# Kernel optimization log

Measured on AMD Instinct MI355X. Metric: run time of the kernel, lower is better.

The kernel has to match this reference:

```python
import jax, jax.numpy as jnp
import numpy as np

EMBED = 1024
HEADS = 16
HEAD_DIM = EMBED // HEADS
HIDDEN = 4096
EPS = 1e-5


def setup_inputs() -> dict:
    key = jax.random.key(0)
    ks = jax.random.split(key, 16)
    s_e = 1.0 / np.sqrt(EMBED)
    s_h = 1.0 / np.sqrt(HIDDEN)
    return {
        "x": jax.random.normal(ks[0], (8, 1024, EMBED), dtype=jnp.float32),
        "ln1_g": jnp.ones((EMBED,), jnp.float32),
        "ln1_b": jnp.zeros((EMBED,), jnp.float32),
        "ln2_g": jnp.ones((EMBED,), jnp.float32),
        "ln2_b": jnp.zeros((EMBED,), jnp.float32),
        "wq": jax.random.uniform(ks[1], (EMBED, EMBED), jnp.float32, -s_e, s_e),
        "bq": jax.random.uniform(ks[2], (EMBED,), jnp.float32, -s_e, s_e),
        "wk": jax.random.uniform(ks[3], (EMBED, EMBED), jnp.float32, -s_e, s_e),
        "bk": jax.random.uniform(ks[4], (EMBED,), jnp.float32, -s_e, s_e),
        "wv": jax.random.uniform(ks[5], (EMBED, EMBED), jnp.float32, -s_e, s_e),
        "bv": jax.random.uniform(ks[6], (EMBED,), jnp.float32, -s_e, s_e),
        "wo": jax.random.uniform(ks[7], (EMBED, EMBED), jnp.float32, -s_e, s_e),
        "bo": jax.random.uniform(ks[8], (EMBED,), jnp.float32, -s_e, s_e),
        "w1": jax.random.uniform(ks[9], (EMBED, HIDDEN), jnp.float32, -s_e, s_e),
        "b1": jax.random.uniform(ks[10], (HIDDEN,), jnp.float32, -s_e, s_e),
        "w2": jax.random.uniform(ks[11], (HIDDEN, EMBED), jnp.float32, -s_h, s_h),
        "b2": jax.random.uniform(ks[12], (EMBED,), jnp.float32, -s_h, s_h),
    }


def _layernorm(x, g, b):
    mu = jnp.mean(x, axis=-1, keepdims=True)
    var = jnp.mean((x - mu) ** 2, axis=-1, keepdims=True)
    return (x - mu) * jax.lax.rsqrt(var + EPS) * g + b


def reference(x, ln1_g, ln1_b, ln2_g, ln2_b, wq, bq, wk, bk, wv, bv, wo, bo, w1, b1, w2, b2):
    B, N, E = x.shape
    scale = HEAD_DIM ** (-0.5)
    # --- attention sublayer (pre-norm) ---
    h = _layernorm(x, ln1_g, ln1_b)
    q = (h @ wq + bq).reshape(B, N, HEADS, HEAD_DIM).transpose(0, 2, 1, 3) * scale
    k = (h @ wk + bk).reshape(B, N, HEADS, HEAD_DIM).transpose(0, 2, 1, 3)
    v = (h @ wv + bv).reshape(B, N, HEADS, HEAD_DIM).transpose(0, 2, 1, 3)
    scores = jnp.einsum("bhqd,bhkd->bhqk", q, k)
    attn = jax.nn.softmax(scores, axis=-1)
    ctx = jnp.einsum("bhqk,bhkd->bhqd", attn, v)
    ctx = ctx.transpose(0, 2, 1, 3).reshape(B, N, E)
    x = x + (ctx @ wo + bo)
    # --- FFN sublayer (pre-norm) ---
    h2 = _layernorm(x, ln2_g, ln2_b)
    ff = jax.nn.relu(h2 @ w1 + b1) @ w2 + b2
    return x + ff
```

## Files before the change

### kernel.cpp

```cpp
#include <hip/hip_runtime.h>
#include <hip/hip_bf16.h>

typedef __attribute__((ext_vector_type(4))) float f32x4;
typedef __attribute__((ext_vector_type(16))) float f32x16;
typedef __attribute__((ext_vector_type(8))) __bf16 bf16x8;
typedef __attribute__((ext_vector_type(4))) __bf16 bf16x4;
typedef __attribute__((ext_vector_type(4))) unsigned int u32x4;

static constexpr int E    = 1024;
static constexpr int TOK  = 8192;
static constexpr int HID  = 4096;

#define DEVINL __device__ __forceinline__

DEVINL void gload16(const void* g, void* l) {
  __builtin_amdgcn_global_load_lds((__attribute__((address_space(1))) void*)g,
                                   (__attribute__((address_space(3))) void*)l, 16, 0, 0);
}

#define ABAR()  asm volatile("s_barrier" ::: "memory")
#define AVM(n)  asm volatile("s_waitcnt vmcnt(" #n ")" ::: "memory")
#define ALGKM0() asm volatile("s_waitcnt lgkmcnt(0)")
#define CVTPK(dst, lo, hi) asm("v_cvt_pk_bf16_f32 %0, %1, %2" : "=v"(dst) : "v"(lo), "v"(hi))
#define PLSWAP(a, b) asm("v_permlane32_swap_b32 %0, %1" : "+v"(a), "+v"(b))

template <int N> DEVINL void avm() {
  if constexpr (N == 0)      asm volatile("s_waitcnt vmcnt(0)" ::: "memory");
  else if constexpr (N == 2) asm volatile("s_waitcnt vmcnt(2)" ::: "memory");
  else if constexpr (N == 6) asm volatile("s_waitcnt vmcnt(6)" ::: "memory");
  else if constexpr (N == 8) asm volatile("s_waitcnt vmcnt(8)" ::: "memory");
  else if constexpr (N == 9) asm volatile("s_waitcnt vmcnt(9)" ::: "memory");
  else                       asm volatile("s_waitcnt vmcnt(0)" ::: "memory");
}

__global__ __launch_bounds__(256) void wconv6ln_kernel(const float* __restrict__ wq,
                                                       const float* __restrict__ wk,
                                                       const float* __restrict__ wv,
                                                       const float* __restrict__ wo,
                                                       const float* __restrict__ w1,
                                                       const float* __restrict__ w2,
                                                       __bf16* __restrict__ Wqkv,
                                                       __bf16* __restrict__ Wot,
                                                       __bf16* __restrict__ W1t,
                                                       __bf16* __restrict__ W2t,
                                                       const float* __restrict__ X,
                                                       const float* __restrict__ g,
                                                       const float* __restrict__ be,
                                                       __bf16* __restrict__ O) {
  const int id = blockIdx.x;
  const int t  = threadIdx.x;
  __shared__ float tile[32][33];
  __shared__ float red[8];

  if (id >= 12288) {
    const long row = id - 12288;
    float4 v = *(const float4*)&X[row * E + t * 4];
    float s  = v.x + v.y + v.z + v.w;
    float ss = v.x * v.x + v.y * v.y + v.z * v.z + v.w * v.w;
#pragma unroll
    for (int off = 32; off; off >>= 1) {
      s  += __shfl_down(s, off);
      ss += __shfl_down(ss, off);
    }
    const int w = t >> 6;
    if ((t & 63) == 0) { red[w] = s; red[4 + w] = ss; }
    __syncthreads();
    s  = red[0] + red[1] + red[2] + red[3];
    ss = red[4] + red[5] + red[6] + red[7];
    const float mean = s * (1.0f / E);
    const float var  = ss * (1.0f / E) - mean * mean;
    const float rstd = rsqrtf(var + 1e-5f);
    float4 gv = *(const float4*)&g[t * 4];
    float4 bv = *(const float4*)&be[t * 4];
    bf16x4 o;
    o[0] = (__bf16)((v.x - mean) * rstd * gv.x + bv.x);
    o[1] = (__bf16)((v.y - mean) * rstd * gv.y + bv.y);
    o[2] = (__bf16)((v.z - mean) * rstd * gv.z + bv.z);
    o[3] = (__bf16)((v.w - mean) * rstd * gv.w + bv.w);
    *(bf16x4*)&O[row * E + t * 4] = o;
    return;
  }

  const float* W; __bf16* Wt; int K, N, lid;
  if (id < 1024)      { W = wq; Wt = Wqkv;                K = 1024; N = 1024; lid = id; }
  else if (id < 2048) { W = wk; Wt = Wqkv + 1024 * 1024;  K = 1024; N = 1024; lid = id - 1024; }
  else if (id < 3072) { W = wv; Wt = Wqkv + 2048 * 1024;  K = 1024; N = 1024; lid = id - 2048; }
  else if (id < 4096) { W = wo; Wt = Wot;                 K = 1024; N = 1024; lid = id - 3072; }
  else if (id < 8192) { W = w1; Wt = W1t;                 K = 1024; N = 4096; lid = id - 4096; }
  else                { W = w2; Wt = W2t;                 K = 4096; N = 1024; lid = id - 8192; }
  const int nx = N >> 5;
  const long n0 = (long)(lid % nx) * 32;
  const long k0 = (long)(lid / nx) * 32;

  const int r  = t >> 3;
  const int c4 = (t & 7) * 4;
  float4 v = *(const float4*)&W[(k0 + r) * N + n0 + c4];
  tile[r][c4 + 0] = v.x; tile[r][c4 + 1] = v.y;
  tile[r][c4 + 2] = v.z; tile[r][c4 + 3] = v.w;
  __syncthreads();
  bf16x4 o;
#pragma unroll
  for (int i = 0; i < 4; ++i) o[i] = (__bf16)tile[c4 + i][r];
  *(bf16x4*)&Wt[(n0 + r) * K + k0 + c4] = o;
}

__global__ __launch_bounds__(256) void ln_kernel(const float* __restrict__ X,
                                                 const float* __restrict__ g,
                                                 const float* __restrict__ be,
                                                 __bf16* __restrict__ O) {
  const int t = threadIdx.x;
  const long row = blockIdx.x;
  float4 v = *(const float4*)&X[row * E + t * 4];
  float s  = v.x + v.y + v.z + v.w;
  float ss = v.x * v.x + v.y * v.y + v.z * v.z + v.w * v.w;
#pragma unroll
  for (int off = 32; off; off >>= 1) {
    s  += __shfl_down(s, off);
    ss += __shfl_down(ss, off);
  }
  __shared__ float red[8];
  const int w = t >> 6;
  if ((t & 63) == 0) { red[w] = s; red[4 + w] = ss; }
  __syncthreads();
  s  = red[0] + red[1] + red[2] + red[3];
  ss = red[4] + red[5] + red[6] + red[7];
  const float mean = s * (1.0f / E);
  const float var  = ss * (1.0f / E) - mean * mean;
  const float rstd = rsqrtf(var + 1e-5f);
  float4 gv = *(const float4*)&g[t * 4];
  float4 bv = *(const float4*)&be[t * 4];
  bf16x4 o;
  o[0] = (__bf16)((v.x - mean) * rstd * gv.x + bv.x);
  o[1] = (__bf16)((v.y - mean) * rstd * gv.y + bv.y);
  o[2] = (__bf16)((v.z - mean) * rstd * gv.z + bv.z);
  o[3] = (__bf16)((v.w - mean) * rstd * gv.w + bv.w);
  *(bf16x4*)&O[row * E + t * 4] = o;
}

template <bool RELU, bool RESID, bool OUTBF, int NB>
__global__ __launch_bounds__(512, 2) void gemm8p_kernel(const __bf16* __restrict__ A,
                                                        const __bf16* __restrict__ Bt,
                                                        const float* __restrict__ bias0,
                                                        const float* __restrict__ bias1,
                                                        const float* __restrict__ bias2,
                                                        const float* resid,
                                                        void* Cout, void* Cout2,
                                                        int M, int N, int K, int KLD) {
  extern __shared__ char lds[];
  const int tid  = threadIdx.x;
  const int lane = tid & 63;
  const int l15  = lane & 15;
  const int kp   = lane >> 4;
  const int wid  = tid >> 6;
  const int wr   = wid >> 2;
  const int wc   = wid & 3;

  const int gx   = gridDim.x, gy = gridDim.y;
  const int nwg  = gx * gy * gridDim.z;
  const int flat = blockIdx.x + gx * (blockIdx.y + gy * blockIdx.z);
  const int swz  = (flat & 7) * (nwg >> 3) + (flat >> 3);
  const int bx   = swz % gx;
  const int by   = (swz / gx) % gy;
  const int bz   = swz / (gx * gy);
  const long brow = (long)by * 256;
  const long bcol = (long)bx * 256;
  const long koff = (long)bz * K;

  const __bf16* Ab = A  + brow * KLD + koff;
  const __bf16* Bb = Bt + bcol * KLD + koff;
  void* Cdst = bz ? Cout2 : Cout;
  const int NT = K >> 6;

  auto stageU = [&](const __bf16* Gb, int rc0, int k0, int dstOff) {
#pragma unroll
    for (int i = 0; i < 2; ++i) {
      const int c = i * 512 + tid;
      const int r = c >> 3;
      const int p = (c & 7) ^ (r & 7);
      gload16(Gb + (long)(rc0 + r) * KLD + k0 + p * 8, lds + dstOff + c * 16);
    }
  };

  f32x4 acc[8][4];
  const f32x4 z4 = {0.f, 0.f, 0.f, 0.f};
#pragma unroll
  for (int m = 0; m < 8; ++m)
#pragma unroll
    for (int n = 0; n < 4; ++n) acc[m][n] = z4;

  bf16x8 af[4][2], bh0[2][2], bh1[2][2];

  auto readA = [&](int off) {
#pragma unroll
    for (int mm = 0; mm < 4; ++mm)
#pragma unroll
      for (int kk = 0; kk < 2; ++kk) {
        const int lr = mm * 32 + wr * 16 + l15;
        const int p  = ((kk << 2) + kp) ^ (lr & 7);
        af[mm][kk] = *(const bf16x8*)(lds + off + lr * 128 + p * 16);
      }
  };
  auto readB = [&](int off, bf16x8 (*bf)[2]) {
#pragma unroll
    for (int nn = 0; nn < 2; ++nn)
#pragma unroll
      for (int kk = 0; kk < 2; ++kk) {
        const int lc = nn * 64 + wc * 16 + l15;
        const int p  = ((kk << 2) + kp) ^ (lc & 7);
        bf[nn][kk] = *(const bf16x8*)(lds + off + lc * 128 + p * 16);
      }
  };
  auto quad = [&](int mb, int nb, bf16x8 (*bf)[2]) {
    __builtin_amdgcn_s_setprio(1);
#pragma unroll
    for (int kk = 0; kk < 2; ++kk)
#pragma unroll
      for (int mm = 0; mm < 4; ++mm)
#pragma unroll
        for (int nn = 0; nn < 2; ++nn)
          acc[mb + mm][nb + nn] = __builtin_amdgcn_mfma_f32_16x16x32_bf16(
              af[mm][kk], bf[nn][kk], acc[mb + mm][nb + nn], 0, 0, 0);
    __builtin_amdgcn_s_setprio(0);
  };

  stageU(Ab, 0,   0, 0);
  stageU(Bb, 0,   0, 32768);
  stageU(Bb, 128, 0, 49152);
  stageU(Ab, 128, 0, 16384);
  stageU(Ab, 0,   64, 65536 + 0);
  stageU(Bb, 0,   64, 65536 + 32768);
  stageU(Bb, 128, 64, 65536 + 49152);
  avm<6>();
  ABAR();

  for (int t = 0; t < NT; ++t) {
    const int cb  = (t & 1) ? 65536 : 0;
    const int nb1 = cb ^ 65536;
    const int k1 = (t + 1 < NT) ? ((t + 1) << 6) : 0;
    const int k2 = (t + 2 < NT) ? ((t + 2) << 6) : 0;

    readA(cb + 0);
    readB(cb + 32768, bh0);
    stageU(Ab, 128, k1, nb1 + 16384);
    ABAR(); ALGKM0();
    quad(0, 0, bh0);
    ABAR();

    readB(cb + 49152, bh1);
    stageU(Ab, 0, k2, cb + 0);
    ABAR(); ALGKM0();
    quad(0, 2, bh1);
    ABAR();

    readA(cb + 16384);
    stageU(Bb, 0, k2, cb + 32768);
    ABAR(); ALGKM0();
    quad(4, 0, bh0);
    ABAR();

    stageU(Bb, 128, k2, cb + 49152);
    avm<6>();
    ABAR();
    quad(4, 2, bh1);
    ABAR();
  }
  avm<0>();

#pragma unroll
  for (int m = 0; m < 8; ++m) {
#pragma unroll
    for (int n = 0; n < 4; ++n) {
      const long col = bcol + n * 64 + wc * 16 + l15;
      float bb;
      if (NB == 3) {
        const float* bp = (col < 1024) ? bias0 : ((col < 2048) ? bias1 : bias2);
        bb = bp[col & 1023];
      } else if (NB == 1) {
        bb = bias0[col];
      } else {
        bb = 0.f;
      }
#pragma unroll
      for (int j = 0; j < 4; ++j) {
        const long row = brow + m * 32 + wr * 16 + (lane >> 4) * 4 + j;
        float val = acc[m][n][j] + bb;
        if (RELU) val = fmaxf(val, 0.f);
        const long idx = row * N + col;
        if (RESID) val += resid[idx];
        if (OUTBF) ((__bf16*)Cdst)[idx] = (__bf16)val;
        else       ((float*)Cdst)[idx]  = val;
      }
    }
  }
}

template <int BM_, int DEPTH, bool RELU, bool RESID, bool OUTBF, int NB>
__global__ __launch_bounds__(512, 2) void gemmk_kernel(const __bf16* __restrict__ A,
                                                       const __bf16* __restrict__ Bt,
                                                       const float* __restrict__ bias0,
                                                       const float* __restrict__ bias1,
                                                       const float* __restrict__ bias2,
                                                       const float* resid,
                                                       void* Cout, void* Cout2,
                                                       int M, int N, int K, int KLD) {
  extern __shared__ char lds[];
  constexpr int MF    = BM_ / 32;
  constexpr int ABYT  = BM_ * 64;
  constexpr int TILEB = ABYT + 16384;
  constexpr int AL    = BM_ / 128;
  constexpr int TL    = AL + 2;
  constexpr int W     = (DEPTH - 2) * TL;

  const int tid  = threadIdx.x;
  const int lane = tid & 63;
  const int l15  = lane & 15;
  const int kp   = lane >> 4;
  const int wid  = tid >> 6;
  const int wr   = wid >> 2;
  const int wc   = wid & 3;

  const int gx   = gridDim.x, gy = gridDim.y;
  const int nwg  = gx * gy * gridDim.z;
  const int flat = blockIdx.x + gx * (blockIdx.y + gy * blockIdx.z);
  const int swz  = (flat & 7) * (nwg >> 3) + (flat >> 3);
  const int bx   = swz % gx;
  const int by   = (swz / gx) % gy;
  const int bz   = swz / (gx * gy);
  const long brow = (long)by * BM_;
  const long bcol = (long)bx * 256;
  const long koff = (long)bz * K;

  const __bf16* Ab = A  + brow * KLD + koff;
  const __bf16* Bb = Bt + bcol * KLD + koff;
  void* Cdst = bz ? Cout2 : Cout;
  const int NT = K >> 5;

  auto stageA = [&](int k0, char* dst) {
#pragma unroll
    for (int i = 0; i < AL; ++i) {
      const int c = i * 512 + tid;
      const int r = c >> 2;
      const int p = (c & 3) ^ ((r >> 1) & 3);
      gload16(Ab + (long)r * KLD + k0 + p * 8, dst + c * 16);
    }
  };
  auto stageB = [&](int k0, char* dst) {
#pragma unroll
    for (int i = 0; i < 2; ++i) {
      const int c = i * 512 + tid;
      const int r = c >> 2;
      const int p = (c & 3) ^ ((r >> 1) & 3);
      gload16(Bb + (long)r * KLD + k0 + p * 8, dst + c * 16);
    }
  };

  f32x4 acc[MF][4];
  const f32x4 z4 = {0.f, 0.f, 0.f, 0.f};
#pragma unroll
  for (int m = 0; m < MF; ++m)
#pragma unroll
    for (int n = 0; n < 4; ++n) acc[m][n] = z4;

#pragma unroll
  for (int pt = 0; pt < DEPTH - 1; ++pt) {
    stageA(pt * 32, lds + pt * TILEB);
    stageB(pt * 32, lds + pt * TILEB + ABYT);
  }

  bf16x8 af[4], bfr[4];

  for (int t = 0; t < NT; ++t) {
    const int cb = t % DEPTH;
    const int sb = (t + DEPTH - 1) % DEPTH;
    const char* Ac = lds + cb * TILEB;
    const char* Bc = Ac + ABYT;
    char* An = lds + sb * TILEB;
    const int kt = (t + DEPTH - 1 < NT) ? ((t + DEPTH - 1) << 5) : 0;

    avm<W>();
    ABAR();

#pragma unroll
    for (int m = 0; m < 4; ++m) {
      const int row = m * 32 + wr * 16 + l15;
      af[m] = *(const bf16x8*)(Ac + row * 64 + (kp ^ ((row >> 1) & 3)) * 16);
    }
#pragma unroll
    for (int n = 0; n < 4; ++n) {
      const int col = n * 64 + wc * 16 + l15;
      bfr[n] = *(const bf16x8*)(Bc + col * 64 + (kp ^ ((col >> 1) & 3)) * 16);
    }
    stageA(kt, An);
    stageB(kt, An + ABYT);
    __builtin_amdgcn_s_setprio(1);
#pragma unroll
    for (int m = 0; m < 4; ++m)
#pragma unroll
      for (int n = 0; n < 4; ++n)
        acc[m][n] = __builtin_amdgcn_mfma_f32_16x16x32_bf16(af[m], bfr[n], acc[m][n], 0, 0, 0);
    __builtin_amdgcn_s_setprio(0);
  }
  avm<0>();

#pragma unroll
  for (int m = 0; m < MF; ++m) {
#pragma unroll
    for (int n = 0; n < 4; ++n) {
      const long col = bcol + n * 64 + wc * 16 + l15;
      float bb;
      if (NB == 3) {
        const float* bp = (col < 1024) ? bias0 : ((col < 2048) ? bias1 : bias2);
        bb = bp[col & 1023];
      } else if (NB == 1) {
        bb = bias0[col];
      } else {
        bb = 0.f;
      }
#pragma unroll
      for (int j = 0; j < 4; ++j) {
        const long row = brow + m * 32 + wr * 16 + (lane >> 4) * 4 + j;
        float val = acc[m][n][j] + bb;
        if (RELU) val = fmaxf(val, 0.f);
        const long idx = row * N + col;
        if (RESID) val += resid[idx];
        if (OUTBF) ((__bf16*)Cdst)[idx] = (__bf16)val;
        else       ((float*)Cdst)[idx]  = val;
      }
    }
  }
}

__global__ __launch_bounds__(256, 3) void attn_kernel(const __bf16* __restrict__ QKV,
                                                      __bf16* __restrict__ Og) {
  __shared__ __align__(16) __bf16 Qs[128 * 64];
  __shared__ __align__(16) __bf16 Ks[2][64 * 64];
  __shared__ __align__(16) __bf16 Vt[2][64 * 64];

  const int QSTR = 3072;
  const int t    = threadIdx.x;
  const int lane = t & 63;
  const int w    = t >> 6;
  const int l31  = lane & 31;
  const int h    = lane >> 5;
  const int b    = blockIdx.y >> 4;
  const int hh   = blockIdx.y & 15;
  const long row0 = (long)b * 1024 + (long)blockIdx.x * 128;
  const long kvrow0 = (long)b * 1024;
  const int colQ = hh * 64;
  const int colK = colQ + 1024;
  const int colV = colQ + 2048;

#pragma unroll
  for (int j = 0; j < 4; ++j) {
    const int c = j * 256 + t;
    const int r = c >> 3;
    const int p = (c & 7) ^ (r & 7);
    gload16(QKV + (row0 + r) * QSTR + colQ + p * 8, (char*)Qs + c * 16);
  }
#pragma unroll
  for (int j = 0; j < 2; ++j) {
    const int c = j * 256 + t;
    const int r = c >> 3;
    const int p = (c & 7) ^ (r & 7);
    gload16(QKV + (kvrow0 + r) * QSTR + colK + p * 8, (char*)Ks[0] + c * 16);
  }
  bf16x8 vv[2];
#pragma unroll
  for (int j = 0; j < 2; ++j) {
    const int c = j * 256 + t;
    const int key = c >> 3, dc = c & 7;
    vv[j] = *(const bf16x8*)(QKV + (kvrow0 + key) * QSTR + colV + dc * 8);
  }
  AVM(0);
#pragma unroll
  for (int j = 0; j < 2; ++j) {
    const int c = j * 256 + t;
    const int key = c >> 3, dc = c & 7;
#pragma unroll
    for (int e = 0; e < 8; ++e) {
      const int d = dc * 8 + e;
      *(__bf16*)((char*)Vt[0] + d * 128 + (((key >> 3) ^ dc) * 16) + (key & 7) * 2) = vv[j][e];
    }
  }
  __syncthreads();

  bf16x8 bq[4];
  {
    const int qrow = w * 32 + l31;
#pragma unroll
    for (int kk = 0; kk < 4; ++kk) {
      const int p = (kk * 2 + h) ^ (qrow & 7);
      bq[kk] = *(const bf16x8*)((const char*)Qs + qrow * 128 + p * 16);
    }
  }

  f32x16 ctx0, ctx1;
#pragma unroll
  for (int r = 0; r < 16; ++r) { ctx0[r] = 0.f; ctx1[r] = 0.f; }
  float m = -INFINITY, l = 0.f;

  for (int kb = 0; kb < 16; ++kb) {
    const int cur = kb & 1, nxt = cur ^ 1;
    const int kb1 = (kb + 1 < 16) ? kb + 1 : kb;
    const long kr1 = kvrow0 + kb1 * 64;

#pragma unroll
    for (int j = 0; j < 2; ++j) {
      const int c = j * 256 + t;
      const int key = c >> 3, dc = c & 7;
      vv[j] = *(const bf16x8*)(QKV + (kr1 + key) * QSTR + colV + dc * 8);
    }
#pragma unroll
    for (int j = 0; j < 2; ++j) {
      const int c = j * 256 + t;
      const int r = c >> 3;
      const int p = (c & 7) ^ (r & 7);
      gload16(QKV + (kr1 + r) * QSTR + colK + p * 8, (char*)Ks[nxt] + c * 16);
    }

    f32x16 s0, s1;
#pragma unroll
    for (int r = 0; r < 16; ++r) { s0[r] = 0.f; s1[r] = 0.f; }
    __builtin_amdgcn_s_setprio(1);
#pragma unroll
    for (int kk = 0; kk < 4; ++kk) {
      const int pce = kk * 2 + h;
      const int p0i = pce ^ (l31 & 7);
      bf16x8 ak0 = *(const bf16x8*)((const char*)Ks[cur] + l31 * 128 + p0i * 16);
      bf16x8 ak1 = *(const bf16x8*)((const char*)Ks[cur] + (32 + l31) * 128 + p0i * 16);
      s0 = __builtin_amdgcn_mfma_f32_32x32x16_bf16(ak0, bq[kk], s0, 0, 0, 0);
      s1 = __builtin_amdgcn_mfma_f32_32x32x16_bf16(ak1, bq[kk], s1, 0, 0, 0);
    }
    __builtin_amdgcn_s_setprio(0);

    float mx = s0[0];
#pragma unroll
    for (int r = 1; r < 16; ++r) mx = fmaxf(mx, s0[r]);
#pragma unroll
    for (int r = 0; r < 16; ++r) mx = fmaxf(mx, s1[r]);
    mx = fmaxf(mx, __shfl_xor(mx, 32));

    if (!__all(mx - m <= 64.f)) {
      const float mn = fmaxf(m, mx);
      const float corr = __expf((m - mn) * 0.125f);
      l *= corr;
#pragma unroll
      for (int r = 0; r < 16; ++r) { ctx0[r] *= corr; ctx1[r] *= corr; }
      m = mn;
    }
    f32x16 p0, p1;
    float rs = 0.f;
#pragma unroll
    for (int r = 0; r < 16; ++r) { p0[r] = __expf((s0[r] - m) * 0.125f); rs += p0[r]; }
#pragma unroll
    for (int r = 0; r < 16; ++r) { p1[r] = __expf((s1[r] - m) * 0.125f); rs += p1[r]; }
    rs += __shfl_xor(rs, 32);
    l += rs;

    AVM(2);
#pragma unroll
    for (int j = 0; j < 2; ++j) {
      const int c = j * 256 + t;
      const int key = c >> 3, dc = c & 7;
#pragma unroll
      for (int e = 0; e < 8; ++e) {
        const int d = dc * 8 + e;
        *(__bf16*)((char*)Vt[nxt] + d * 128 + (((key >> 3) ^ dc) * 16) + (key & 7) * 2) = vv[j][e];
      }
    }

    bf16x8 paf[4];
#pragma unroll
    for (int ks = 0; ks < 4; ++ks) {
      const int base = (ks & 1) * 8;
      unsigned a0, a1, b0, b1;
      if (ks < 2) {
        CVTPK(a0, p0[base + 0], p0[base + 1]);
        CVTPK(b0, p0[base + 4], p0[base + 5]);
        CVTPK(a1, p0[base + 2], p0[base + 3]);
        CVTPK(b1, p0[base + 6], p0[base + 7]);
      } else {
        CVTPK(a0, p1[base + 0], p1[base + 1]);
        CVTPK(b0, p1[base + 4], p1[base + 5]);
        CVTPK(a1, p1[base + 2], p1[base + 3]);
        CVTPK(b1, p1[base + 6], p1[base + 7]);
      }
      PLSWAP(a0, b0);
      PLSWAP(a1, b1);
      u32x4 wv4; wv4[0] = a0; wv4[1] = a1; wv4[2] = b0; wv4[3] = b1;
      paf[ks] = __builtin_bit_cast(bf16x8, wv4);
    }

    __builtin_amdgcn_s_setprio(1);
#pragma unroll
    for (int ks = 0; ks < 4; ++ks) {
      const int pce = ks * 2 + h;
      bf16x8 av0 = *(const bf16x8*)((const char*)Vt[cur] + l31 * 128 + ((pce ^ (l31 >> 3)) * 16));
      bf16x8 av1 = *(const bf16x8*)((const char*)Vt[cur] + (32 + l31) * 128 + ((pce ^ (4 + (l31 >> 3))) * 16));
      ctx0 = __builtin_amdgcn_mfma_f32_32x32x16_bf16(av0, paf[ks], ctx0, 0, 0, 0);
      ctx1 = __builtin_amdgcn_mfma_f32_32x32x16_bf16(av1, paf[ks], ctx1, 0, 0, 0);
    }
    __builtin_amdgcn_s_setprio(0);

    __syncthreads();
  }

  const float inv = 1.0f / l;
  const long orow = row0 + w * 32 + l31;
#pragma unroll
  for (int f = 0; f < 2; ++f)
#pragma unroll
    for (int tq = 0; tq < 4; ++tq) {
      bf16x4 o;
#pragma unroll
      for (int e = 0; e < 4; ++e) {
        const float v = (f ? ctx1[tq * 4 + e] : ctx0[tq * 4 + e]) * inv;
        o[e] = (__bf16)v;
      }
      const int col = colQ + f * 32 + tq * 8 + h * 4;
      *(bf16x4*)&Og[orow * E + col] = o;
    }
}

extern "C" void kernel_launch(void* const* d_in, const int* in_sizes, int n_in,
                              void* d_out, int out_size, void* d_ws, size_t ws_size,
                              hipStream_t stream) {
  const float* x     = (const float*)d_in[0];
  const float* ln1g  = (const float*)d_in[1];
  const float* ln1b  = (const float*)d_in[2];
  const float* ln2g  = (const float*)d_in[3];
  const float* ln2b  = (const float*)d_in[4];
  const float* wq    = (const float*)d_in[5];
  const float* bq    = (const float*)d_in[6];
  const float* wk    = (const float*)d_in[7];
  const float* bk    = (const float*)d_in[8];
  const float* wv    = (const float*)d_in[9];
  const float* bv    = (const float*)d_in[10];
  const float* wo    = (const float*)d_in[11];
  const float* bo    = (const float*)d_in[12];
  const float* w1    = (const float*)d_in[13];
  const float* b1    = (const float*)d_in[14];
  const float* w2    = (const float*)d_in[15];
  const float* b2    = (const float*)d_in[16];
  float* out = (float*)d_out;

  char* ws = (char*)d_ws;
  const size_t MB = 1024 * 1024;
  __bf16* Wqkv = (__bf16*)(ws + 0 * MB);
  __bf16* Wot  = (__bf16*)(ws + 6 * MB);
  __bf16* W1t  = (__bf16*)(ws + 8 * MB);
  __bf16* W2t  = (__bf16*)(ws + 16 * MB);
  __bf16* h    = (__bf16*)(ws + 24 * MB);
  __bf16* qkv  = (__bf16*)(ws + 40 * MB);
  __bf16* ctx  = (__bf16*)(ws + 88 * MB);
  __bf16* ff1  = (__bf16*)(ws + 40 * MB);

  const dim3 blk(256);
  const dim3 blk512(512);
  const size_t GLDS8P  = 131072;
  const size_t GLDS128 = 5 * (128 * 64 + 16384);

  wconv6ln_kernel<<<20480, blk, 0, stream>>>(wq, wk, wv, wo, w1, w2,
                                             Wqkv, Wot, W1t, W2t,
                                             x, ln1g, ln1b, h);

  gemm8p_kernel<false, false, true, 3><<<dim3(3072 / 256, TOK / 256), blk512, GLDS8P, stream>>>(
      h, Wqkv, bq, bk, bv, nullptr, qkv, nullptr, TOK, 3072, E, E);

  attn_kernel<<<dim3(8, 128), blk, 0, stream>>>(qkv, ctx);

  gemmk_kernel<128, 5, false, true, false, 1><<<dim3(E / 256, TOK / 128), blk512, GLDS128, stream>>>(
      ctx, Wot, bo, nullptr, nullptr, x, out, nullptr, TOK, E, E, E);

  ln_kernel<<<TOK, blk, 0, stream>>>(out, ln2g, ln2b, h);

  gemm8p_kernel<true, false, true, 1><<<dim3(HID / 256, TOK / 256), blk512, GLDS8P, stream>>>(
      h, W1t, b1, nullptr, nullptr, nullptr, ff1, nullptr, TOK, HID, E, E);

  gemmk_kernel<128, 5, false, true, false, 1><<<dim3(E / 256, TOK / 128), blk512, GLDS128, stream>>>(
      ff1, W2t, b2, nullptr, nullptr, out, out, nullptr, TOK, E, HID, HID);
}
```

Baseline: 350.8 us.

## Replace gemmk with 128x256 eight-phase double-buffered GEMM using BK=64 quadrant schedule

Result: no change. 352.5 us (+0.5%).

```diff
diff --git a/kernel.cpp b/kernel.cpp
--- a/kernel.cpp
+++ b/kernel.cpp
@@ -27,9 +27,8 @@
 template <int N> DEVINL void avm() {
   if constexpr (N == 0)      asm volatile("s_waitcnt vmcnt(0)" ::: "memory");
   else if constexpr (N == 2) asm volatile("s_waitcnt vmcnt(2)" ::: "memory");
+  else if constexpr (N == 5) asm volatile("s_waitcnt vmcnt(5)" ::: "memory");
   else if constexpr (N == 6) asm volatile("s_waitcnt vmcnt(6)" ::: "memory");
-  else if constexpr (N == 8) asm volatile("s_waitcnt vmcnt(8)" ::: "memory");
-  else if constexpr (N == 9) asm volatile("s_waitcnt vmcnt(9)" ::: "memory");
   else                       asm volatile("s_waitcnt vmcnt(0)" ::: "memory");
 }
 
@@ -144,7 +143,7 @@
                                                         const float* __restrict__ bias1,
                                                         const float* __restrict__ bias2,
                                                         const float* resid,
-                                                        void* Cout, void* Cout2,
+                                                        void* Cout,
                                                         int M, int N, int K, int KLD) {
   extern __shared__ char lds[];
   const int tid  = threadIdx.x;
@@ -156,19 +155,16 @@
   const int wc   = wid & 3;
 
   const int gx   = gridDim.x, gy = gridDim.y;
-  const int nwg  = gx * gy * gridDim.z;
-  const int flat = blockIdx.x + gx * (blockIdx.y + gy * blockIdx.z);
+  const int nwg  = gx * gy;
+  const int flat = blockIdx.x + gx * blockIdx.y;
   const int swz  = (flat & 7) * (nwg >> 3) + (flat >> 3);
   const int bx   = swz % gx;
-  const int by   = (swz / gx) % gy;
-  const int bz   = swz / (gx * gy);
+  const int by   = swz / gx;
   const long brow = (long)by * 256;
   const long bcol = (long)bx * 256;
-  const long koff = (long)bz * K;
-
-  const __bf16* Ab = A  + brow * KLD + koff;
-  const __bf16* Bb = Bt + bcol * KLD + koff;
-  void* Cdst = bz ? Cout2 : Cout;
+
+  const __bf16* Ab = A  + brow * KLD;
+  const __bf16* Bb = Bt + bcol * KLD;
   const int NT = K >> 6;
 
   auto stageU = [&](const __bf16* Gb, int rc0, int k0, int dstOff) {
@@ -287,30 +283,23 @@
         if (RELU) val = fmaxf(val, 0.f);
         const long idx = row * N + col;
         if (RESID) val += resid[idx];
-        if (OUTBF) ((__bf16*)Cdst)[idx] = (__bf16)val;
-        else       ((float*)Cdst)[idx]  = val;
+        if (OUTBF) ((__bf16*)Cout)[idx] = (__bf16)val;
+        else       ((float*)Cout)[idx]  = val;
       }
     }
   }
 }
 
-template <int BM_, int DEPTH, bool RELU, bool RESID, bool OUTBF, int NB>
-__global__ __launch_bounds__(512, 2) void gemmk_kernel(const __bf16* __restrict__ A,
-                                                       const __bf16* __restrict__ Bt,
-                                                       const float* __restrict__ bias0,
-                                                       const float* __restrict__ bias1,
-                                                       const float* __restrict__ bias2,
-                                                       const float* resid,
-                                                       void* Cout, void* Cout2,
-                                                       int M, int N, int K, int KLD) {
+template <bool RELU, bool RESID, bool OUTBF, int NB>
+__global__ __launch_bounds__(512, 2) void gemm8h_kernel(const __bf16* __restrict__ A,
+                                                        const __bf16* __restrict__ Bt,
+                                                        const float* __restrict__ bias0,
+                                                        const float* __restrict__ bias1,
+                                                        const float* __restrict__ bias2,
+                                                        const float* resid,
+                                                        void* Cout,
+                                                        int M, int N, int K, int KLD) {
   extern __shared__ char lds[];
-  constexpr int MF    = BM_ / 32;
-  constexpr int ABYT  = BM_ * 64;
-  constexpr int TILEB = ABYT + 16384;
-  constexpr int AL    = BM_ / 128;
-  constexpr int TL    = AL + 2;
-  constexpr int W     = (DEPTH - 2) * TL;
-
   const int tid  = threadIdx.x;
   const int lane = tid & 63;
   const int l15  = lane & 15;
@@ -320,90 +309,121 @@
   const int wc   = wid & 3;
 
   const int gx   = gridDim.x, gy = gridDim.y;
-  const int nwg  = gx * gy * gridDim.z;
-  const int flat = blockIdx.x + gx * (blockIdx.y + gy * blockIdx.z);
+  const int nwg  = gx * gy;
+  const int flat = blockIdx.x + gx * blockIdx.y;
   const int swz  = (flat & 7) * (nwg >> 3) + (flat >> 3);
   const int bx   = swz % gx;
-  const int by   = (swz / gx) % gy;
-  const int bz   = swz / (gx * gy);
-  const long brow = (long)by * BM_;
+  const int by   = swz / gx;
+  const long brow = (long)by * 128;
   const long bcol = (long)bx * 256;
-  const long koff = (long)bz * K;
-
-  const __bf16* Ab = A  + brow * KLD + koff;
-  const __bf16* Bb = Bt + bcol * KLD + koff;
-  void* Cdst = bz ? Cout2 : Cout;
-  const int NT = K >> 5;
-
-  auto stageA = [&](int k0, char* dst) {
-#pragma unroll
-    for (int i = 0; i < AL; ++i) {
-      const int c = i * 512 + tid;
-      const int r = c >> 2;
-      const int p = (c & 3) ^ ((r >> 1) & 3);
-      gload16(Ab + (long)r * KLD + k0 + p * 8, dst + c * 16);
-    }
-  };
-  auto stageB = [&](int k0, char* dst) {
+
+  const __bf16* Ab = A  + brow * KLD;
+  const __bf16* Bb = Bt + bcol * KLD;
+  const int NT = K >> 6;
+
+  auto stageA = [&](int rc0, int k0, int dstOff) {
+    const int c = tid;
+    const int r = c >> 3;
+    const int p = (c & 7) ^ (r & 7);
+    gload16(Ab + (long)(rc0 + r) * KLD + k0 + p * 8, lds + dstOff + c * 16);
+  };
+  auto stageB = [&](int rc0, int k0, int dstOff) {
 #pragma unroll
     for (int i = 0; i < 2; ++i) {
       const int c = i * 512 + tid;
-      const int r = c >> 2;
-      const int p = (c & 3) ^ ((r >> 1) & 3);
-      gload16(Bb + (long)r * KLD + k0 + p * 8, dst + c * 16);
-    }
-  };
-
-  f32x4 acc[MF][4];
+      const int r = c >> 3;
+      const int p = (c & 7) ^ (r & 7);
+      gload16(Bb + (long)(rc0 + r) * KLD + k0 + p * 8, lds + dstOff + c * 16);
+    }
+  };
+
+  f32x4 acc[4][4];
   const f32x4 z4 = {0.f, 0.f, 0.f, 0.f};
 #pragma unroll
-  for (int m = 0; m < MF; ++m)
+  for (int m = 0; m < 4; ++m)
 #pragma unroll
     for (int n = 0; n < 4; ++n) acc[m][n] = z4;
 
-#pragma unroll
-  for (int pt = 0; pt < DEPTH - 1; ++pt) {
-    stageA(pt * 32, lds + pt * TILEB);
-    stageB(pt * 32, lds + pt * TILEB + ABYT);
-  }
-
-  bf16x8 af[4], bfr[4];
+  bf16x8 af[2][2], bh0[2][2], bh1[2][2];
+
+  auto readA = [&](int off) {
+#pragma unroll
+    for (int mm = 0; mm < 2; ++mm)
+#pragma unroll
+      for (int kk = 0; kk < 2; ++kk) {
+        const int lr = mm * 32 + wr * 16 + l15;
+        const int p  = ((kk << 2) + kp) ^ (lr & 7);
+        af[mm][kk] = *(const bf16x8*)(lds + off + lr * 128 + p * 16);
+      }
+  };
+  auto readB = [&](int off, bf16x8 (*bf)[2]) {
+#pragma unroll
+    for (int nn = 0; nn < 2; ++nn)
+#pragma unroll
+      for (int kk = 0; kk < 2; ++kk) {
+        const int lc = nn * 64 + wc * 16 + l15;
+        const int p  = ((kk << 2) + kp) ^ (lc & 7);
+        bf[nn][kk] = *(const bf16x8*)(lds + off + lc * 128 + p * 16);
+      }
+  };
+  auto quad = [&](int mb, int nb, bf16x8 (*bf)[2]) {
+    __builtin_amdgcn_s_setprio(1);
+#pragma unroll
+    for (int kk = 0; kk < 2; ++kk)
+#pragma unroll
+      for (int mm = 0; mm < 2; ++mm)
+#pragma unroll
+        for (int nn = 0; nn < 2; ++nn)
+          acc[mb + mm][nb + nn] = __builtin_amdgcn_mfma_f32_16x16x32_bf16(
+              af[mm][kk], bf[nn][kk], acc[mb + mm][nb + nn], 0, 0, 0);
+    __builtin_amdgcn_s_setprio(0);
+  };
+
+  stageA(0,   0, 0);
+  stageB(0,   0, 16384);
+  stageB(128, 0, 32768);
+  stageA(64,  0, 8192);
+  stageA(0,   64, 49152 + 0);
+  stageB(0,   64, 49152 + 16384);
+  stageB(128, 64, 49152 + 32768);
+  avm<5>();
+  ABAR();
 
   for (int t = 0; t < NT; ++t) {
-    const int cb = t % DEPTH;
-    const int sb = (t + DEPTH - 1) % DEPTH;
-    const char* Ac = lds + cb * TILEB;
-    const char* Bc = Ac + ABYT;
-    char* An = lds + sb * TILEB;
-    const int kt = (t + DEPTH - 1 < NT) ? ((t + DEPTH - 1) << 5) : 0;
-
-    avm<W>();
-    ABAR();
-
-#pragma unroll
-    for (int m = 0; m < 4; ++m) {
-      const int row = m * 32 + wr * 16 + l15;
-      af[m] = *(const bf16x8*)(Ac + row * 64 + (kp ^ ((row >> 1) & 3)) * 16);
-    }
-#pragma unroll
-    for (int n = 0; n < 4; ++n) {
-      const int col = n * 64 + wc * 16 + l15;
-      bfr[n] = *(const bf16x8*)(Bc + col * 64 + (kp ^ ((col >> 1) & 3)) * 16);
-    }
-    stageA(kt, An);
-    stageB(kt, An + ABYT);
-    __builtin_amdgcn_s_setprio(1);
-#pragma unroll
-    for (int m = 0; m < 4; ++m)
-#pragma unroll
-      for (int n = 0; n < 4; ++n)
-        acc[m][n] = __builtin_amdgcn_mfma_f32_16x16x32_bf16(af[m], bfr[n], acc[m][n], 0, 0, 0);
-    __builtin_amdgcn_s_setprio(0);
+    const int cb  = (t & 1) ? 49152 : 0;
+    const int nb1 = cb ^ 49152;
+    const int k1 = (t + 1 < NT) ? ((t + 1) << 6) : 0;
+    const int k2 = (t + 2 < NT) ? ((t + 2) << 6) : 0;
+
+    readA(cb + 0);
+    readB(cb + 16384, bh0);
+    stageA(64, k1, nb1 + 8192);
+    ABAR(); ALGKM0();
+    quad(0, 0, bh0);
+    ABAR();
+
+    readB(cb + 32768, bh1);
+    stageA(0, k2, cb + 0);
+    ABAR(); ALGKM0();
+    quad(0, 2, bh1);
+    ABAR();
+
+    readA(cb + 8192);
+    stageB(0, k2, cb + 16384);
+    ABAR(); ALGKM0();
+    quad(2, 0, bh0);
+    ABAR();
+
+    stageB(128, k2, cb + 32768);
+    avm<5>();
+    ABAR();
+    quad(2, 2, bh1);
+    ABAR();
   }
   avm<0>();
 
 #pragma unroll
-  for (int m = 0; m < MF; ++m) {
+  for (int m = 0; m < 4; ++m) {
 #pragma unroll
     for (int n = 0; n < 4; ++n) {
       const long col = bcol + n * 64 + wc * 16 + l15;
@@ -423,8 +443,8 @@
         if (RELU) val = fmaxf(val, 0.f);
         const long idx = row * N + col;
         if (RESID) val += resid[idx];
-        if (OUTBF) ((__bf16*)Cdst)[idx] = (__bf16)val;
-        else       ((float*)Cdst)[idx]  = val;
+        if (OUTBF) ((__bf16*)Cout)[idx] = (__bf16)val;
+        else       ((float*)Cout)[idx]  = val;
       }
     }
   }
@@ -657,26 +677,26 @@
 
   const dim3 blk(256);
   const dim3 blk512(512);
-  const size_t GLDS8P  = 131072;
-  const size_t GLDS128 = 5 * (128 * 64 + 16384);
+  const size_t GLDS8P = 131072;
+  const size_t GLDS8H = 98304;
 
   wconv6ln_kernel<<<20480, blk, 0, stream>>>(wq, wk, wv, wo, w1, w2,
                                              Wqkv, Wot, W1t, W2t,
                                              x, ln1g, ln1b, h);
 
-  gemm8p_kernel<false, false, true, 3><<<dim3(3072 / 256, TOK / 256), blk512, GLDS8P, stream>>>(
-      h, Wqkv, bq, bk, bv, nullptr, qkv, nullptr, TOK, 3072, E, E);
+  gemm8h_kernel<false, false, true, 3><<<dim3(3072 / 256, TOK / 128), blk512, GLDS8H, stream>>>(
+      h, Wqkv, bq, bk, bv, nullptr, qkv, TOK, 3072, E, E);
 
   attn_kernel<<<dim3(8, 128), blk, 0, stream>>>(qkv, ctx);
 
-  gemmk_kernel<128, 5, false, true, false, 1><<<dim3(E / 256, TOK / 128), blk512, GLDS128, stream>>>(
-      ctx, Wot, bo, nullptr, nullptr, x, out, nullptr, TOK, E, E, E);
+  gemm8h_kernel<false, true, false, 1><<<dim3(E / 256, TOK / 128), blk512, GLDS8H, stream>>>(
+      ctx, Wot, bo, nullptr, nullptr, x, out, TOK, E, E, E);
 
   ln_kernel<<<TOK, blk, 0, stream>>>(out, ln2g, ln2b, h);
 
   gemm8p_kernel<true, false, true, 1><<<dim3(HID / 256, TOK / 256), blk512, GLDS8P, stream>>>(
-      h, W1t, b1, nullptr, nullptr, nullptr, ff1, nullptr, TOK, HID, E, E);
-
-  gemmk_kernel<128, 5, false, true, false, 1><<<dim3(E / 256, TOK / 128), blk512, GLDS128, stream>>>(
-      ff1, W2t, b2, nullptr, nullptr, out, out, nullptr, TOK, E, HID, HID);
+      h, W1t, b1, nullptr, nullptr, nullptr, ff1, TOK, HID, E, E);
+
+  gemm8h_kernel<false, true, false, 1><<<dim3(E / 256, TOK / 128), blk512, GLDS8H, stream>>>(
+      ff1, W2t, b2, nullptr, nullptr, out, out, TOK, E, HID, HID);
 }
```
